# Performance work log

Measured on AMD Instinct MI355X. Metric: run time of the kernel, lower is better.

The kernel has to match this reference:

```python
import jax, jax.numpy as jnp
import numpy as np

B, T, C = 2, 2048, 1024
H, HS = 16, 64
THETA = 10000.0


def _rope_tables(seq_len, dim, dtype):
    inv_freq = 1.0 / (THETA ** (jnp.arange(0, dim, 2, dtype=jnp.float32) / dim))
    t = jnp.arange(seq_len, dtype=jnp.float32)
    freqs = t[:, None] * inv_freq[None, :]          # [T, dim/2]
    emb = jnp.concatenate([freqs, freqs], axis=-1)  # [T, dim]
    return jnp.cos(emb).astype(dtype), jnp.sin(emb).astype(dtype)


def _rotate_half(x):
    x1, x2 = jnp.split(x, 2, axis=-1)
    return jnp.concatenate([-x2, x1], axis=-1)


def setup_inputs() -> dict:
    key = jax.random.key(0)
    ks = jax.random.split(key, 9)
    s = 0.02
    return {
        "q_x": jax.random.normal(ks[0], (B, T, C), dtype=jnp.float32),
        "wq": jax.random.normal(ks[1], (C, H * HS), dtype=jnp.float32) * s,
        "bq": jnp.zeros((H * HS,), dtype=jnp.float32),
        "wk": jax.random.normal(ks[2], (C, H * HS), dtype=jnp.float32) * s,
        "bk": jnp.zeros((H * HS,), dtype=jnp.float32),
        "wv": jax.random.normal(ks[3], (C, H * HS), dtype=jnp.float32) * s,
        "bv": jnp.zeros((H * HS,), dtype=jnp.float32),
        "wc": jax.random.normal(ks[4], (H * HS, C), dtype=jnp.float32) * s,
        "bc": jnp.zeros((C,), dtype=jnp.float32),
    }


def reference(q_x, wq, bq, wk, bk, wv, bv, wc, bc):
    b, t, _ = q_x.shape
    # Q/K/V projections -> [B, H, T, HS]
    q = (q_x @ wq + bq).reshape(b, t, H, HS).transpose(0, 2, 1, 3)
    k = (q_x @ wk + bk).reshape(b, t, H, HS).transpose(0, 2, 1, 3)
    v = (q_x @ wv + bv).reshape(b, t, H, HS).transpose(0, 2, 1, 3)
    # RoPE (concat-half rotation)
    cos, sin = _rope_tables(t, HS, q.dtype)  # [T, HS]
    q = q * cos + _rotate_half(q) * sin
    k = k * cos + _rotate_half(k) * sin
    # Naive causal attention
    scale = 1.0 / np.sqrt(HS)
    att = jnp.einsum("bhqd,bhkd->bhqk", q, k) * scale
    mask = jnp.tril(jnp.ones((t, t), dtype=bool))
    att = jnp.where(mask, att, -jnp.inf)
    att = jax.nn.softmax(att, axis=-1)
    y = jnp.einsum("bhqk,bhkd->bhqd", att, v)
    y = y.transpose(0, 2, 1, 3).reshape(b, t, H * HS)
    return y @ wc + bc
```

## Files before the change

### kernel.cpp

```cpp
#include <hip/hip_runtime.h>

#define B_  2
#define T_  2048
#define C_  1024
#define H_  16
#define HS_ 64
#define M_  4096
#define N_  1024
#define K_  1024

typedef float floatx4 __attribute__((ext_vector_type(4)));
typedef short bf16x8  __attribute__((ext_vector_type(8)));

__device__ __forceinline__ float bf2f(unsigned short u) {
    return __uint_as_float(((unsigned int)u) << 16);
}
__device__ __forceinline__ unsigned short f2bf(float f) {
    unsigned int u = __float_as_uint(f);
    return (unsigned short)((u + 0x7fffu + ((u >> 16) & 1u)) >> 16);
}
__device__ __forceinline__ unsigned int pack2(float a, float b) {
    return (unsigned int)f2bf(a) | ((unsigned int)f2bf(b) << 16);
}
__device__ __forceinline__ unsigned int pack2t(float a, float b) {
    return __builtin_amdgcn_perm(__float_as_uint(b), __float_as_uint(a), 0x07060302u);
}
__device__ __forceinline__ void async16(const unsigned short* g, unsigned short* l) {
    __builtin_amdgcn_global_load_lds(
        (const __attribute__((address_space(1))) unsigned int*)g,
        (__attribute__((address_space(3))) unsigned int*)l, 16, 0, 0);
}

__global__ __launch_bounds__(256) void prep_kernel(
    const float* __restrict__ x,
    const float* __restrict__ w0, const float* __restrict__ w1,
    const float* __restrict__ w2, const float* __restrict__ w3,
    unsigned short* __restrict__ xb, unsigned short* __restrict__ wTall)
{
    __shared__ float tile[64][65];
    const int bid = blockIdx.x;
    const int t = threadIdx.x;
    if (bid < 4096) {
        const size_t i = ((size_t)bid * 256 + t) * 4;
        const float4 v = *(const float4*)(x + i);
        ushort4 st;
        st.x = f2bf(v.x); st.y = f2bf(v.y); st.z = f2bf(v.z); st.w = f2bf(v.w);
        *(ushort4*)(xb + i) = st;
        return;
    }
    const int zb = bid - 4096;
    const int z = zb >> 8, rem = zb & 255;
    const float* w = (z == 0) ? w0 : (z == 1) ? w1 : (z == 2) ? w2 : w3;
    unsigned short* wT = wTall + ((size_t)z << 20);
    const int n0 = (rem & 15) * 64, k0 = (rem >> 4) * 64;

    const int r = t >> 2, cq = (t & 3) * 16;
    const float4* src = (const float4*)(w + (size_t)(k0 + r) * N_ + n0 + cq);
    const float4 v0 = src[0], v1 = src[1], v2 = src[2], v3 = src[3];
    tile[r][cq+0]=v0.x; tile[r][cq+1]=v0.y; tile[r][cq+2]=v0.z; tile[r][cq+3]=v0.w;
    tile[r][cq+4]=v1.x; tile[r][cq+5]=v1.y; tile[r][cq+6]=v1.z; tile[r][cq+7]=v1.w;
    tile[r][cq+8]=v2.x; tile[r][cq+9]=v2.y; tile[r][cq+10]=v2.z; tile[r][cq+11]=v2.w;
    tile[r][cq+12]=v3.x; tile[r][cq+13]=v3.y; tile[r][cq+14]=v3.z; tile[r][cq+15]=v3.w;
    __syncthreads();

    const int rn = t >> 2, ck = (t & 3) * 16;
    unsigned int o[8];
#pragma unroll
    for (int ii = 0; ii < 8; ii++)
        o[ii] = pack2(tile[ck + 2*ii][rn], tile[ck + 2*ii + 1][rn]);
    unsigned short* dst = wT + (size_t)(n0 + rn) * K_ + k0 + ck;
    *(uint4*)dst       = make_uint4(o[0], o[1], o[2], o[3]);
    *(uint4*)(dst + 8) = make_uint4(o[4], o[5], o[6], o[7]);
}

__global__ __launch_bounds__(512, 2) void qkv_gemm(
    const unsigned short* __restrict__ xb, const unsigned short* __restrict__ wT,
    const float* __restrict__ bq, const float* __restrict__ bk,
    const float* __restrict__ bv,
    unsigned short* __restrict__ qb, unsigned short* __restrict__ kb,
    unsigned short* __restrict__ vb)
{
    __shared__ unsigned short lds[65536];

    const int tid  = threadIdx.x;
    const int lane = tid & 63;
    const int wave = tid >> 6;

    const int bid = blockIdx.x;
    const int swz = (bid & 7) * 24 + (bid >> 3);
    const int nb  = swz % 12;
    const int mb  = swz / 12;
    const int m0  = mb * 256;
    const int n0g = nb * 256;

    const int wm = wave >> 2, wn = wave & 3;
    const int fr = lane & 15, quad = lane >> 4;

    const int r_s = tid >> 2;
    const int c_s = (tid & 3) ^ ((tid >> 3) & 3);
    const unsigned short* aS0 = xb + (size_t)(m0 + r_s) * 1024 + c_s * 8;
    const unsigned short* aS1 = aS0 + (size_t)128 * 1024;
    const unsigned short* bS0 = wT + (size_t)(n0g + r_s) * 1024 + c_s * 8;
    const unsigned short* bS1 = bS0 + (size_t)128 * 1024;
    unsigned short* ldw = &lds[wave * 512];

    auto stage = [&](int buf, int region, const unsigned short* s0,
                     const unsigned short* s1) {
        unsigned short* d = ldw + buf * 32768 + region * 8192;
        async16(s0, d);
        async16(s1, d + 4096);
    };

    int oA[8], oB[4];
#pragma unroll
    for (int i = 0; i < 8; i++) {
        const int r = wm * 128 + i * 16 + fr;
        oA[i] = r * 32 + ((quad ^ ((r >> 1) & 3)) << 3);
    }
#pragma unroll
    for (int j = 0; j < 4; j++) {
        const int r = wn * 64 + j * 16 + fr;
        oB[j] = r * 32 + ((quad ^ ((r >> 1) & 3)) << 3);
    }

    floatx4 acc[8][4];
#pragma unroll
    for (int i = 0; i < 8; i++)
#pragma unroll
        for (int j = 0; j < 4; j++) acc[i][j] = (floatx4){0.f, 0.f, 0.f, 0.f};

    stage(0, 0, aS0,      aS1);
    stage(0, 2, bS0,      bS1);
    stage(0, 1, aS0 + 32, aS1 + 32);
    stage(0, 3, bS0 + 32, bS1 + 32);
    stage(1, 0, aS0 + 64, aS1 + 64);
    stage(1, 2, bS0 + 64, bS1 + 64);
    asm volatile("s_waitcnt vmcnt(8)" ::: "memory");
    __builtin_amdgcn_s_barrier();
    __builtin_amdgcn_sched_barrier(0);

    bf16x8 af[4], bfr[4];
#pragma unroll 2
    for (int t = 0; t < 16; ++t) {
        const int cur = t & 1, nxt = cur ^ 1;
        const unsigned short* A0 = &lds[cur * 32768];
        const unsigned short* A1 = A0 + 8192;
        const unsigned short* B0 = A0 + 16384;
        const unsigned short* B1 = A0 + 24576;
        const int k1 = (t + 1) * 64, k2 = (t + 2) * 64;

#pragma unroll
        for (int i = 0; i < 4; i++) af[i]  = *(const bf16x8*)&A0[oA[i]];
#pragma unroll
        for (int j = 0; j < 4; j++) bfr[j] = *(const bf16x8*)&B0[oB[j]];
        if (t + 1 < 16) stage(nxt, 1, aS0 + k1 + 32, aS1 + k1 + 32);
        __builtin_amdgcn_s_barrier();
        asm volatile("s_waitcnt lgkmcnt(0)" ::: "memory");
        __builtin_amdgcn_s_setprio(1);
#pragma unroll
        for (int i = 0; i < 4; i++)
#pragma unroll
            for (int j = 0; j < 4; j++)
                acc[i][j] = __builtin_amdgcn_mfma_f32_16x16x32_bf16(
                    af[i], bfr[j], acc[i][j], 0, 0, 0);
        __builtin_amdgcn_s_setprio(0);
        __builtin_amdgcn_s_barrier();
        __builtin_amdgcn_sched_barrier(0);

#pragma unroll
        for (int i = 0; i < 4; i++) af[i] = *(const bf16x8*)&A0[oA[4 + i]];
        if (t + 1 < 16) stage(nxt, 3, bS0 + k1 + 32, bS1 + k1 + 32);
        if (t < 15) { asm volatile("s_waitcnt vmcnt(8)" ::: "memory"); }
        else        { asm volatile("s_waitcnt vmcnt(0)" ::: "memory"); }
        __builtin_amdgcn_s_barrier();
        asm volatile("s_waitcnt lgkmcnt(0)" ::: "memory");
        __builtin_amdgcn_s_setprio(1);
#pragma unroll
        for (int i = 0; i < 4; i++)
#pragma unroll
            for (int j = 0; j < 4; j++)
                acc[4 + i][j] = __builtin_amdgcn_mfma_f32_16x16x32_bf16(
                    af[i], bfr[j], acc[4 + i][j], 0, 0, 0);
        __builtin_amdgcn_s_setprio(0);
        __builtin_amdgcn_s_barrier();
        __builtin_amdgcn_sched_barrier(0);

#pragma unroll
        for (int i = 0; i < 4; i++) af[i]  = *(const bf16x8*)&A1[oA[i]];
#pragma unroll
        for (int j = 0; j < 4; j++) bfr[j] = *(const bf16x8*)&B1[oB[j]];
        if (t + 2 < 16) stage(cur, 0, aS0 + k2, aS1 + k2);
        __builtin_amdgcn_s_barrier();
        asm volatile("s_waitcnt lgkmcnt(0)" ::: "memory");
        __builtin_amdgcn_s_setprio(1);
#pragma unroll
        for (int i = 0; i < 4; i++)
#pragma unroll
            for (int j = 0; j < 4; j++)
                acc[i][j] = __builtin_amdgcn_mfma_f32_16x16x32_bf16(
                    af[i], bfr[j], acc[i][j], 0, 0, 0);
        __builtin_amdgcn_s_setprio(0);
        __builtin_amdgcn_s_barrier();
        __builtin_amdgcn_sched_barrier(0);

#pragma unroll
        for (int i = 0; i < 4; i++) af[i] = *(const bf16x8*)&A1[oA[4 + i]];
        if (t + 2 < 16) stage(cur, 2, bS0 + k2, bS1 + k2);
        if (t < 14) { asm volatile("s_waitcnt vmcnt(8)" ::: "memory"); }
        else        { asm volatile("s_waitcnt vmcnt(0)" ::: "memory"); }
        __builtin_amdgcn_s_barrier();
        asm volatile("s_waitcnt lgkmcnt(0)" ::: "memory");
        __builtin_amdgcn_s_setprio(1);
#pragma unroll
        for (int i = 0; i < 4; i++)
#pragma unroll
            for (int j = 0; j < 4; j++)
                acc[4 + i][j] = __builtin_amdgcn_mfma_f32_16x16x32_bf16(
                    af[i], bfr[j], acc[4 + i][j], 0, 0, 0);
        __builtin_amdgcn_s_setprio(0);
        __builtin_amdgcn_s_barrier();
        __builtin_amdgcn_sched_barrier(0);
    }

    const int p = nb >> 2;
    const int colbase = (nb & 3) * 256 + wn * 64;
    const int h = colbase >> 6;
    const int rb = quad * 4;
    const float* bias = (p == 0) ? bq : (p == 1) ? bk : bv;

    if (p == 2) {
#pragma unroll
        for (int j = 0; j < 4; j++) {
            const int d = j * 16 + fr;
            const float bz = bias[colbase + d];
#pragma unroll
            for (int i = 0; i < 8; i++) {
                const int row0 = m0 + wm * 128 + i * 16 + rb;
                const int bb = row0 >> 11, tt = row0 & 2047;
                ushort4 st;
                st.x = f2bf(acc[i][j][0] + bz);
                st.y = f2bf(acc[i][j][1] + bz);
                st.z = f2bf(acc[i][j][2] + bz);
                st.w = f2bf(acc[i][j][3] + bz);
                *(ushort4*)&vb[((size_t)(bb * H_ + h) * HS_ + d) * T_ + tt] = st;
            }
        }
    } else {
        unsigned short* out = (p == 0) ? qb : kb;
        const float qsc = (p == 0) ? 0.18033688011111772f : 1.0f;
        const float bz0 = bias[colbase + fr];
        const float bz1 = bias[colbase + 16 + fr];
        const float bz2 = bias[colbase + 32 + fr];
        const float bz3 = bias[colbase + 48 + fr];
        const float nl = -0.41524101186279297f;
        const float if0 = exp2f((float)fr * nl);
        const float if1 = exp2f((float)(fr + 16) * nl);
#pragma unroll
        for (int i = 0; i < 8; i++) {
#pragma unroll
            for (int pr = 0; pr < 4; pr++) {
                const int row = m0 + wm * 128 + i * 16 + rb + pr;
                const int bb = row >> 11, tt = row & 2047;
                float s0, c0, s1, c1;
                __sincosf((float)tt * if0, &s0, &c0);
                __sincosf((float)tt * if1, &s1, &c1);
                const float v0 = acc[i][0][pr] + bz0;
                const float v1 = acc[i][1][pr] + bz1;
                const float v2 = acc[i][2][pr] + bz2;
                const float v3 = acc[i][3][pr] + bz3;
                unsigned short* ob = out + ((size_t)(bb * H_ + h) * T_ + tt) * HS_ + fr;
                ob[0]  = f2bf((v0 * c0 - v2 * s0) * qsc);
                ob[16] = f2bf((v1 * c1 - v3 * s1) * qsc);
                ob[32] = f2bf((v2 * c0 + v0 * s0) * qsc);
                ob[48] = f2bf((v3 * c1 + v1 * s1) * qsc);
            }
        }
    }
}

__global__ __launch_bounds__(256) void attn_kernel(
    const unsigned short* __restrict__ qb, const unsigned short* __restrict__ kb,
    const unsigned short* __restrict__ vt, unsigned short* __restrict__ yb,
    unsigned short* __restrict__ Opart, float* __restrict__ Mpart)
{
    __shared__ unsigned short Ks[2][64 * 64];
    __shared__ unsigned short Vs[2][64 * 64];
    __shared__ unsigned short Ps[4][16 * 64];

    const int bh = blockIdx.x;
    const int b = bh >> 4, h = bh & 15;
    const int s = 47 - (int)blockIdx.y;
    int qt, ktlo, kthi, half;
    bool split;
    if (s < 16) { qt = s; ktlo = 0; kthi = qt; half = 0; split = false; }
    else {
        const int idx = s - 16;
        qt = 16 + (idx >> 1); half = idx & 1;
        const int nf = (qt + 2) >> 1;
        ktlo = half ? nf : 0;
        kthi = half ? qt : nf - 1;
        split = true;
    }
    const int r0 = qt * 64;
    const int tid  = threadIdx.x;
    const int lane = tid & 63;
    const int wave = tid >> 6;
    const int l4   = lane & 15;
    const int quad = lane >> 4;

    const int qrow_g = r0 + wave * 16 + l4;

    bf16x8 qf[2];
    {
        const unsigned short* qp = qb + ((size_t)bh * T_ + qrow_g) * HS_ + quad * 8;
        qf[0] = *(const bf16x8*)(qp);
        qf[1] = *(const bf16x8*)(qp + 32);
    }

    floatx4 o[4];
#pragma unroll
    for (int g = 0; g < 4; g++) o[g] = (floatx4){0.f, 0.f, 0.f, 0.f};
    float m = -1e30f, l = 0.f;

    const int srow = tid >> 2;
    const int sc16 = (tid & 3) * 16;
    const int ssw  = (srow & 7) * 8;
    const int psw  = (l4 & 7) * 8;

    const unsigned short* kp = kb + ((size_t)bh * T_ + srow) * HS_ + sc16;
    const unsigned short* vp = vt + ((size_t)(bh * 64 + srow)) * T_ + sc16;

    uint4 rk0 = *(const uint4*)(kp + (size_t)ktlo * 64 * HS_);
    uint4 rk1 = *(const uint4*)(kp + (size_t)ktlo * 64 * HS_ + 8);
    uint4 rv0 = *(const uint4*)(vp + ktlo * 64);
    uint4 rv1 = *(const uint4*)(vp + ktlo * 64 + 8);
    *(uint4*)&Ks[0][srow * 64 + ( sc16      ^ ssw)] = rk0;
    *(uint4*)&Ks[0][srow * 64 + ((sc16 + 8) ^ ssw)] = rk1;
    *(uint4*)&Vs[0][srow * 64 + ( sc16      ^ ssw)] = rv0;
    *(uint4*)&Vs[0][srow * 64 + ((sc16 + 8) ^ ssw)] = rv1;

    for (int kt = ktlo; kt <= kthi; kt++) {
        const int cur = (kt - ktlo) & 1;
        if (kt < kthi) {
            const unsigned short* kpn = kp + (size_t)(kt + 1) * (64 * HS_);
            const unsigned short* vpn = vp + (kt + 1) * 64;
            rk0 = *(const uint4*)kpn;
            rk1 = *(const uint4*)(kpn + 8);
            rv0 = *(const uint4*)vpn;
            rv1 = *(const uint4*)(vpn + 8);
        }
        __syncthreads();

        floatx4 sf[4];
        __builtin_amdgcn_s_setprio(1);
#pragma unroll
        for (int mg = 0; mg < 4; mg++) {
            const int key = mg * 16 + l4;
            const int ksw = (key & 7) * 8;
            const bf16x8 a0 = *(const bf16x8*)&Ks[cur][key * 64 + ( (quad * 8)       ^ ksw)];
            const bf16x8 a1 = *(const bf16x8*)&Ks[cur][key * 64 + (((quad * 8) + 32) ^ ksw)];
            floatx4 z = (floatx4){0.f, 0.f, 0.f, 0.f};
            z = __builtin_amdgcn_mfma_f32_16x16x32_bf16(a0, qf[0], z, 0, 0, 0);
            z = __builtin_amdgcn_mfma_f32_16x16x32_bf16(a1, qf[1], z, 0, 0, 0);
            sf[mg] = z;
        }
        __builtin_amdgcn_s_setprio(0);

        if (kt == qt) {
#pragma unroll
            for (int mg = 0; mg < 4; mg++)
#pragma unroll
                for (int r = 0; r < 4; r++)
                    if (kt * 64 + 16 * mg + quad * 4 + r > qrow_g)
                        sf[mg][r] = -1e30f;
        }

        float mx[4];
#pragma unroll
        for (int mg = 0; mg < 4; mg++)
            mx[mg] = fmaxf(fmaxf(sf[mg][0], sf[mg][1]),
                           fmaxf(sf[mg][2], sf[mg][3]));
        float tm = fmaxf(fmaxf(mx[0], mx[1]), fmaxf(mx[2], mx[3]));

        if (!__all(tm <= m + 8.f)) {
            tm = fmaxf(tm, __shfl_xor(tm, 16));
            tm = fmaxf(tm, __shfl_xor(tm, 32));
            const float mnew  = fmaxf(m, tm);
            const float alpha = __builtin_amdgcn_exp2f(m - mnew);
            l *= alpha;
#pragma unroll
            for (int g = 0; g < 4; g++) o[g] = o[g] * alpha;
            m = mnew;
        }

        float p[4][4];
        float psg[4];
#pragma unroll
        for (int mg = 0; mg < 4; mg++) {
#pragma unroll
            for (int r = 0; r < 4; r++)
                p[mg][r] = __builtin_amdgcn_exp2f(sf[mg][r] - m);
            psg[mg] = (p[mg][0] + p[mg][1]) + (p[mg][2] + p[mg][3]);
        }
        l += (psg[0] + psg[1]) + (psg[2] + psg[3]);

#pragma unroll
        for (int mg = 0; mg < 4; mg++) {
            const int kb4 = 16 * mg + quad * 4;
            const int off = ((kb4 & ~7) ^ psw) | (kb4 & 7);
            uint2 w;
            w.x = pack2t(p[mg][0], p[mg][1]);
            w.y = pack2t(p[mg][2], p[mg][3]);
            *(uint2*)&Ps[wave][l4 * 64 + off] = w;
        }

        const bf16x8 pf0 = *(const bf16x8*)&Ps[wave][l4 * 64 + ( (quad * 8)       ^ psw)];
        const bf16x8 pf1 = *(const bf16x8*)&Ps[wave][l4 * 64 + (((quad * 8) + 32) ^ psw)];
        __builtin_amdgcn_s_setprio(1);
#pragma unroll
        for (int g = 0; g < 4; g++) {
            const int vd  = g * 16 + l4;
            const int vsw = (vd & 7) * 8;
            const bf16x8 va0 = *(const bf16x8*)&Vs[cur][vd * 64 + ( (quad * 8)       ^ vsw)];
            const bf16x8 va1 = *(const bf16x8*)&Vs[cur][vd * 64 + (((quad * 8) + 32) ^ vsw)];
            o[g] = __builtin_amdgcn_mfma_f32_16x16x32_bf16(va0, pf0, o[g], 0, 0, 0);
            o[g] = __builtin_amdgcn_mfma_f32_16x16x32_bf16(va1, pf1, o[g], 0, 0, 0);
        }
        __builtin_amdgcn_s_setprio(0);

        if (kt < kthi) {
            const int nxt = cur ^ 1;
            *(uint4*)&Ks[nxt][srow * 64 + ( sc16      ^ ssw)] = rk0;
            *(uint4*)&Ks[nxt][srow * 64 + ((sc16 + 8) ^ ssw)] = rk1;
            *(uint4*)&Vs[nxt][srow * 64 + ( sc16      ^ ssw)] = rv0;
            *(uint4*)&Vs[nxt][srow * 64 + ((sc16 + 8) ^ ssw)] = rv1;
        }
    }

    l += __shfl_xor(l, 16);
    l += __shfl_xor(l, 32);

    if (!split) {
        const float invl = 1.f / l;
        unsigned short* yrow = yb + ((size_t)(b * T_ + qrow_g) * H_ + h) * HS_;
#pragma unroll
        for (int g = 0; g < 4; g++) {
            ushort4 st;
            st.x = f2bf(o[g][0] * invl);
            st.y = f2bf(o[g][1] * invl);
            st.z = f2bf(o[g][2] * invl);
            st.w = f2bf(o[g][3] * invl);
            *(ushort4*)&yrow[16 * g + quad * 4] = st;
        }
    } else {
        const int u  = (bh * 16 + (qt - 16)) * 2 + half;
        const int rl = wave * 16 + l4;
        unsigned short* Op = Opart + (size_t)u * 4096 + rl * 64;
#pragma unroll
        for (int g = 0; g < 4; g++) {
            ushort4 st;
            st.x = f2bf(o[g][0]);
            st.y = f2bf(o[g][1]);
            st.z = f2bf(o[g][2]);
            st.w = f2bf(o[g][3]);
            *(ushort4*)&Op[16 * g + quad * 4] = st;
        }
        if (quad == 0) {
            float* ml = Mpart + (size_t)u * 128;
            ml[rl]      = m;
            ml[64 + rl] = l;
        }
    }
}

__global__ __launch_bounds__(256) void attn_combine(
    const unsigned short* __restrict__ Opart, const float* __restrict__ Mpart,
    unsigned short* __restrict__ yb)
{
    const int u  = blockIdx.x;
    const int bh = u >> 4, qt = 16 + (u & 15);
    const int b = bh >> 4, h = bh & 15;
    const int t = threadIdx.x;
    const int r = t >> 2, c = (t & 3) * 16;

    const float* ml1 = Mpart + (size_t)(u * 2) * 128;
    const float* ml2 = ml1 + 128;
    const float m1 = ml1[r], l1 = ml1[64 + r];
    const float m2 = ml2[r], l2 = ml2[64 + r];
    const float M  = fmaxf(m1, m2);
    const float w1 = __builtin_amdgcn_exp2f(m1 - M);
    const float w2 = __builtin_amdgcn_exp2f(m2 - M);
    const float inv = 1.f / (l1 * w1 + l2 * w2);
    const float a1 = w1 * inv, a2 = w2 * inv;

    const unsigned short* O1 = Opart + (size_t)(u * 2)     * 4096 + r * 64 + c;
    const unsigned short* O2 = Opart + (size_t)(u * 2 + 1) * 4096 + r * 64 + c;
    unsigned short* yrow = yb + ((size_t)(b * T_ + qt * 64 + r) * H_ + h) * HS_ + c;

#pragma unroll
    for (int j = 0; j < 2; j++) {
        const uint4 u1 = *(const uint4*)(O1 + 8 * j);
        const uint4 u2 = *(const uint4*)(O2 + 8 * j);
        const unsigned int a[4] = {u1.x, u1.y, u1.z, u1.w};
        const unsigned int d[4] = {u2.x, u2.y, u2.z, u2.w};
        unsigned int ov[4];
#pragma unroll
        for (int q = 0; q < 4; q++) {
            const float y0 = bf2f((unsigned short)(a[q] & 0xffff)) * a1
                           + bf2f((unsigned short)(d[q] & 0xffff)) * a2;
            const float y1 = bf2f((unsigned short)(a[q] >> 16)) * a1
                           + bf2f((unsigned short)(d[q] >> 16)) * a2;
            ov[q] = pack2(y0, y1);
        }
        *(uint4*)(yrow + 8 * j) = make_uint4(ov[0], ov[1], ov[2], ov[3]);
    }
}

__global__ __launch_bounds__(256, 2) void out_gemm(
    const unsigned short* __restrict__ A, const unsigned short* __restrict__ wcT,
    const float* __restrict__ bias, float* __restrict__ out)
{
    __shared__ unsigned short lds[32768];

    const int tid  = threadIdx.x;
    const int lane = tid & 63;
    const int wave = tid >> 6;

    const int bid = blockIdx.x;
    const int swz = (bid & 7) * 32 + (bid >> 3);
    const int nt  = swz >> 5;
    const int mt  = swz & 31;
    const int m0  = mt * 128;
    const int n0  = nt * 128;

    const int wm = wave >> 1, wn = wave & 1;
    const int fr = lane & 15, quad = lane >> 4;

    const int r_s = tid >> 2;
    const int c_s = (tid & 3) ^ ((tid >> 3) & 3);
    const unsigned short* aS0 = A   + (size_t)(m0 + r_s) * 1024 + c_s * 8;
    const unsigned short* aS1 = aS0 + (size_t)64 * 1024;
    const unsigned short* bS0 = wcT + (size_t)(n0 + r_s) * 1024 + c_s * 8;
    const unsigned short* bS1 = bS0 + (size_t)64 * 1024;
    unsigned short* ldw = &lds[wave * 512];

    auto stage = [&](int buf, int region, const unsigned short* s0,
                     const unsigned short* s1) {
        unsigned short* d = ldw + buf * 16384 + region * 4096;
        async16(s0, d);
        async16(s1, d + 2048);
    };

    int oA[4], oB[4];
#pragma unroll
    for (int i = 0; i < 4; i++) {
        const int r = wm * 64 + i * 16 + fr;
        oA[i] = r * 32 + ((quad ^ ((r >> 1) & 3)) << 3);
    }
#pragma unroll
    for (int j = 0; j < 4; j++) {
        const int r = wn * 64 + j * 16 + fr;
        oB[j] = r * 32 + ((quad ^ ((r >> 1) & 3)) << 3);
    }

    floatx4 acc[4][4];
#pragma unroll
    for (int i = 0; i < 4; i++)
#pragma unroll
        for (int j = 0; j < 4; j++) acc[i][j] = (floatx4){0.f, 0.f, 0.f, 0.f};

    stage(0, 0, aS0,      aS1);
    stage(0, 2, bS0,      bS1);
    stage(0, 1, aS0 + 32, aS1 + 32);
    stage(0, 3, bS0 + 32, bS1 + 32);
    stage(1, 0, aS0 + 64, aS1 + 64);
    stage(1, 2, bS0 + 64, bS1 + 64);
    asm volatile("s_waitcnt vmcnt(8)" ::: "memory");
    __builtin_amdgcn_s_barrier();
    __builtin_amdgcn_sched_barrier(0);

    bf16x8 af[2], bfr[4];
#pragma unroll 2
    for (int t = 0; t < 16; ++t) {
        const int cur = t & 1, nxt = cur ^ 1;
        const unsigned short* A0 = &lds[cur * 16384];
        const unsigned short* A1 = A0 + 4096;
        const unsigned short* B0 = A0 + 8192;
        const unsigned short* B1 = A0 + 12288;
        const int k1 = (t + 1) * 64, k2 = (t + 2) * 64;

#pragma unroll
        for (int i = 0; i < 2; i++) af[i]  = *(const bf16x8*)&A0[oA[i]];
#pragma unroll
        for (int j = 0; j < 4; j++) bfr[j] = *(const bf16x8*)&B0[oB[j]];
        if (t + 1 < 16) stage(nxt, 1, aS0 + k1 + 32, aS1 + k1 + 32);
        __builtin_amdgcn_s_barrier();
        asm volatile("s_waitcnt lgkmcnt(0)" ::: "memory");
        __builtin_amdgcn_s_setprio(1);
#pragma unroll
        for (int i = 0; i < 2; i++)
#pragma unroll
            for (int j = 0; j < 4; j++)
                acc[i][j] = __builtin_amdgcn_mfma_f32_16x16x32_bf16(
                    af[i], bfr[j], acc[i][j], 0, 0, 0);
        __builtin_amdgcn_s_setprio(0);
        __builtin_amdgcn_s_barrier();
        __builtin_amdgcn_sched_barrier(0);

#pragma unroll
        for (int i = 0; i < 2; i++) af[i] = *(const bf16x8*)&A0[oA[2 + i]];
        if (t + 1 < 16) stage(nxt, 3, bS0 + k1 + 32, bS1 + k1 + 32);
        if (t < 15) { asm volatile("s_waitcnt vmcnt(8)" ::: "memory"); }
        else        { asm volatile("s_waitcnt vmcnt(0)" ::: "memory"); }
        __builtin_amdgcn_s_barrier();
        asm volatile("s_waitcnt lgkmcnt(0)" ::: "memory");
        __builtin_amdgcn_s_setprio(1);
#pragma unroll
        for (int i = 0; i < 2; i++)
#pragma unroll
            for (int j = 0; j < 4; j++)
                acc[2 + i][j] = __builtin_amdgcn_mfma_f32_16x16x32_bf16(
                    af[i], bfr[j], acc[2 + i][j], 0, 0, 0);
        __builtin_amdgcn_s_setprio(0);
        __builtin_amdgcn_s_barrier();
        __builtin_amdgcn_sched_barrier(0);

#pragma unroll
        for (int i = 0; i < 2; i++) af[i]  = *(const bf16x8*)&A1[oA[i]];
#pragma unroll
        for (int j = 0; j < 4; j++) bfr[j] = *(const bf16x8*)&B1[oB[j]];
        if (t + 2 < 16) stage(cur, 0, aS0 + k2, aS1 + k2);
        __builtin_amdgcn_s_barrier();
        asm volatile("s_waitcnt lgkmcnt(0)" ::: "memory");
        __builtin_amdgcn_s_setprio(1);
#pragma unroll
        for (int i = 0; i < 2; i++)
#pragma unroll
            for (int j = 0; j < 4; j++)
                acc[i][j] = __builtin_amdgcn_mfma_f32_16x16x32_bf16(
                    af[i], bfr[j], acc[i][j], 0, 0, 0);
        __builtin_amdgcn_s_setprio(0);
        __builtin_amdgcn_s_barrier();
        __builtin_amdgcn_sched_barrier(0);

#pragma unroll
        for (int i = 0; i < 2; i++) af[i] = *(const bf16x8*)&A1[oA[2 + i]];
        if (t + 2 < 16) stage(cur, 2, bS0 + k2, bS1 + k2);
        if (t < 14) { asm volatile("s_waitcnt vmcnt(8)" ::: "memory"); }
        else        { asm volatile("s_waitcnt vmcnt(0)" ::: "memory"); }
        __builtin_amdgcn_s_barrier();
        asm volatile("s_waitcnt lgkmcnt(0)" ::: "memory");
        __builtin_amdgcn_s_setprio(1);
#pragma unroll
        for (int i = 0; i < 2; i++)
#pragma unroll
            for (int j = 0; j < 4; j++)
                acc[2 + i][j] = __builtin_amdgcn_mfma_f32_16x16x32_bf16(
                    af[i], bfr[j], acc[2 + i][j], 0, 0, 0);
        __builtin_amdgcn_s_setprio(0);
        __builtin_amdgcn_s_barrier();
        __builtin_amdgcn_sched_barrier(0);
    }

    const int rbase = quad * 4;
#pragma unroll
    for (int j = 0; j < 4; j++) {
        const int col = n0 + wn * 64 + j * 16 + fr;
        const float bz = bias[col];
#pragma unroll
        for (int i = 0; i < 4; i++) {
#pragma unroll
            for (int pr = 0; pr < 4; pr++) {
                const int row = m0 + wm * 64 + i * 16 + rbase + pr;
                out[(size_t)row * N_ + col] = acc[i][j][pr] + bz;
            }
        }
    }
}

extern "C" void kernel_launch(void* const* d_in, const int* in_sizes, int n_in,
                              void* d_out, int out_size, void* d_ws, size_t ws_size,
                              hipStream_t stream) {
    const float* x  = (const float*)d_in[0];
    const float* wq = (const float*)d_in[1];
    const float* bq = (const float*)d_in[2];
    const float* wk = (const float*)d_in[3];
    const float* bk = (const float*)d_in[4];
    const float* wv = (const float*)d_in[5];
    const float* bv = (const float*)d_in[6];
    const float* wc = (const float*)d_in[7];
    const float* bc = (const float*)d_in[8];
    float* out = (float*)d_out;

    unsigned short* ws  = (unsigned short*)d_ws;
    unsigned short* qb  = ws;
    unsigned short* kb  = ws + (size_t)4194304;
    unsigned short* vb  = ws + (size_t)8388608;
    unsigned short* yb  = ws + (size_t)12582912;
    unsigned short* xb  = ws + (size_t)16777216;
    unsigned short* wT  = ws + (size_t)20971520;
    unsigned short* wcT = wT + ((size_t)3 << 20);
    unsigned short* Opart = xb;
    float*          Mpart = (float*)wT;

    prep_kernel<<<5120, 256, 0, stream>>>(x, wq, wk, wv, wc, xb, wT);
    qkv_gemm<<<192, 512, 0, stream>>>(xb, wT, bq, bk, bv, qb, kb, vb);
    attn_kernel<<<dim3(32, 48), 256, 0, stream>>>(qb, kb, vb, yb, Opart, Mpart);
    attn_combine<<<512, 256, 0, stream>>>(Opart, Mpart, yb);
    out_gemm<<<256, 256, 0, stream>>>(yb, wcT, bc, out);
}
```

Measured before the change: 188.0 us.

## Widen attention key/value tiles to 128 keys per iteration

Each loop iteration in the attention kernel now stages 128 keys of K and V into shared memory instead of 64. It computes two 64-key score blocks and feeds them through the softmax and PV MFMA in two halves. This halves the number of barrier-synchronised iterations and per-iteration overheads such as the max reduction and rescale check. The split-KV boundaries and the causal diagonal tile index are recomputed for the wider tiles. It doubles shared memory for K/V and register staging, which may reduce occupancy, and it computes more masked work on the diagonal tile.

```diff
diff --git a/kernel.cpp b/kernel.cpp
--- a/kernel.cpp
+++ b/kernel.cpp
@@ -283,8 +283,8 @@
     const unsigned short* __restrict__ vt, unsigned short* __restrict__ yb,
     unsigned short* __restrict__ Opart, float* __restrict__ Mpart)
 {
-    __shared__ unsigned short Ks[2][64 * 64];
-    __shared__ unsigned short Vs[2][64 * 64];
+    __shared__ unsigned short Ks[2][128 * 64];
+    __shared__ unsigned short Vs[2][64 * 128];
     __shared__ unsigned short Ps[4][16 * 64];
 
     const int bh = blockIdx.x;
@@ -292,15 +292,18 @@
     const int s = 47 - (int)blockIdx.y;
     int qt, ktlo, kthi, half;
     bool split;
-    if (s < 16) { qt = s; ktlo = 0; kthi = qt; half = 0; split = false; }
-    else {
+    if (s < 16) {
+        qt = s; ktlo = 0; kthi = ((qt + 2) >> 1) - 1; half = 0; split = false;
+    } else {
         const int idx = s - 16;
         qt = 16 + (idx >> 1); half = idx & 1;
-        const int nf = (qt + 2) >> 1;
+        const int n  = (qt + 2) >> 1;
+        const int nf = (n + 1) >> 1;
         ktlo = half ? nf : 0;
-        kthi = half ? qt : nf - 1;
+        kthi = half ? n - 1 : nf - 1;
         split = true;
     }
+    const int kdiag = ((qt + 2) >> 1) - 1;
     const int r0 = qt * 64;
     const int tid  = threadIdx.x;
     const int lane = tid & 63;
@@ -330,57 +333,82 @@
     const unsigned short* kp = kb + ((size_t)bh * T_ + srow) * HS_ + sc16;
     const unsigned short* vp = vt + ((size_t)(bh * 64 + srow)) * T_ + sc16;
 
-    uint4 rk0 = *(const uint4*)(kp + (size_t)ktlo * 64 * HS_);
-    uint4 rk1 = *(const uint4*)(kp + (size_t)ktlo * 64 * HS_ + 8);
-    uint4 rv0 = *(const uint4*)(vp + ktlo * 64);
-    uint4 rv1 = *(const uint4*)(vp + ktlo * 64 + 8);
-    *(uint4*)&Ks[0][srow * 64 + ( sc16      ^ ssw)] = rk0;
-    *(uint4*)&Ks[0][srow * 64 + ((sc16 + 8) ^ ssw)] = rk1;
-    *(uint4*)&Vs[0][srow * 64 + ( sc16      ^ ssw)] = rv0;
-    *(uint4*)&Vs[0][srow * 64 + ((sc16 + 8) ^ ssw)] = rv1;
+    uint4 rk0, rk1, rk2, rk3, rv0, rv1, rv2, rv3;
+    {
+        const unsigned short* kpt = kp + (size_t)ktlo * (128 * HS_);
+        rk0 = *(const uint4*)(kpt);
+        rk1 = *(const uint4*)(kpt + 8);
+        rk2 = *(const uint4*)(kpt + 64 * HS_);
+        rk3 = *(const uint4*)(kpt + 64 * HS_ + 8);
+        const unsigned short* vpt = vp + ktlo * 128;
+        rv0 = *(const uint4*)(vpt);
+        rv1 = *(const uint4*)(vpt + 8);
+        rv2 = *(const uint4*)(vpt + 64);
+        rv3 = *(const uint4*)(vpt + 72);
+    }
+    *(uint4*)&Ks[0][ srow       * 64 + ( sc16       ^ ssw)] = rk0;
+    *(uint4*)&Ks[0][ srow       * 64 + ((sc16 + 8)  ^ ssw)] = rk1;
+    *(uint4*)&Ks[0][(srow + 64) * 64 + ( sc16       ^ ssw)] = rk2;
+    *(uint4*)&Ks[0][(srow + 64) * 64 + ((sc16 + 8)  ^ ssw)] = rk3;
+    *(uint4*)&Vs[0][ srow * 128 + ( sc16       ^ ssw)] = rv0;
+    *(uint4*)&Vs[0][ srow * 128 + ((sc16 + 8)  ^ ssw)] = rv1;
+    *(uint4*)&Vs[0][ srow * 128 + ((sc16 + 64) ^ ssw)] = rv2;
+    *(uint4*)&Vs[0][ srow * 128 + ((sc16 + 72) ^ ssw)] = rv3;
 
     for (int kt = ktlo; kt <= kthi; kt++) {
         const int cur = (kt - ktlo) & 1;
         if (kt < kthi) {
-            const unsigned short* kpn = kp + (size_t)(kt + 1) * (64 * HS_);
-            const unsigned short* vpn = vp + (kt + 1) * 64;
+            const unsigned short* kpn = kp + (size_t)(kt + 1) * (128 * HS_);
             rk0 = *(const uint4*)kpn;
             rk1 = *(const uint4*)(kpn + 8);
+            rk2 = *(const uint4*)(kpn + 64 * HS_);
+            rk3 = *(const uint4*)(kpn + 64 * HS_ + 8);
+            const unsigned short* vpn = vp + (kt + 1) * 128;
             rv0 = *(const uint4*)vpn;
             rv1 = *(const uint4*)(vpn + 8);
+            rv2 = *(const uint4*)(vpn + 64);
+            rv3 = *(const uint4*)(vpn + 72);
         }
         __syncthreads();
 
-        floatx4 sf[4];
-        __builtin_amdgcn_s_setprio(1);
+        floatx4 sf[2][4];
+        __builtin_amdgcn_s_setprio(1);
+#pragma unroll
+        for (int hh = 0; hh < 2; hh++)
 #pragma unroll
         for (int mg = 0; mg < 4; mg++) {
-            const int key = mg * 16 + l4;
+            const int key = hh * 64 + mg * 16 + l4;
             const int ksw = (key & 7) * 8;
             const bf16x8 a0 = *(const bf16x8*)&Ks[cur][key * 64 + ( (quad * 8)       ^ ksw)];
             const bf16x8 a1 = *(const bf16x8*)&Ks[cur][key * 64 + (((quad * 8) + 32) ^ ksw)];
             floatx4 z = (floatx4){0.f, 0.f, 0.f, 0.f};
             z = __builtin_amdgcn_mfma_f32_16x16x32_bf16(a0, qf[0], z, 0, 0, 0);
             z = __builtin_amdgcn_mfma_f32_16x16x32_bf16(a1, qf[1], z, 0, 0, 0);
-            sf[mg] = z;
-        }
-        __builtin_amdgcn_s_setprio(0);
-
-        if (kt == qt) {
+            sf[hh][mg] = z;
+        }
+        __builtin_amdgcn_s_setprio(0);
+
+        if (kt == kdiag) {
+#pragma unroll
+            for (int hh = 0; hh < 2; hh++)
 #pragma unroll
             for (int mg = 0; mg < 4; mg++)
 #pragma unroll
                 for (int r = 0; r < 4; r++)
-                    if (kt * 64 + 16 * mg + quad * 4 + r > qrow_g)
-                        sf[mg][r] = -1e30f;
-        }
-
-        float mx[4];
+                    if (kt * 128 + hh * 64 + 16 * mg + quad * 4 + r > qrow_g)
+                        sf[hh][mg][r] = -1e30f;
+        }
+
+        float mxg[8];
+#pragma unroll
+        for (int hh = 0; hh < 2; hh++)
 #pragma unroll
         for (int mg = 0; mg < 4; mg++)
-            mx[mg] = fmaxf(fmaxf(sf[mg][0], sf[mg][1]),
-                           fmaxf(sf[mg][2], sf[mg][3]));
-        float tm = fmaxf(fmaxf(mx[0], mx[1]), fmaxf(mx[2], mx[3]));
+            mxg[hh * 4 + mg] = fmaxf(fmaxf(sf[hh][mg][0], sf[hh][mg][1]),
+                                     fmaxf(sf[hh][mg][2], sf[hh][mg][3]));
+        const float m01 = fmaxf(mxg[0], mxg[1]), m23 = fmaxf(mxg[2], mxg[3]);
+        const float m45 = fmaxf(mxg[4], mxg[5]), m67 = fmaxf(mxg[6], mxg[7]);
+        float tm = fmaxf(fmaxf(m01, m23), fmaxf(m45, m67));
 
         if (!__all(tm <= m + 8.f)) {
             tm = fmaxf(tm, __shfl_xor(tm, 16));
@@ -393,47 +421,54 @@
             m = mnew;
         }
 
-        float p[4][4];
-        float psg[4];
-#pragma unroll
-        for (int mg = 0; mg < 4; mg++) {
-#pragma unroll
-            for (int r = 0; r < 4; r++)
-                p[mg][r] = __builtin_amdgcn_exp2f(sf[mg][r] - m);
-            psg[mg] = (p[mg][0] + p[mg][1]) + (p[mg][2] + p[mg][3]);
-        }
-        l += (psg[0] + psg[1]) + (psg[2] + psg[3]);
-
-#pragma unroll
-        for (int mg = 0; mg < 4; mg++) {
-            const int kb4 = 16 * mg + quad * 4;
-            const int off = ((kb4 & ~7) ^ psw) | (kb4 & 7);
-            uint2 w;
-            w.x = pack2t(p[mg][0], p[mg][1]);
-            w.y = pack2t(p[mg][2], p[mg][3]);
-            *(uint2*)&Ps[wave][l4 * 64 + off] = w;
-        }
-
-        const bf16x8 pf0 = *(const bf16x8*)&Ps[wave][l4 * 64 + ( (quad * 8)       ^ psw)];
-        const bf16x8 pf1 = *(const bf16x8*)&Ps[wave][l4 * 64 + (((quad * 8) + 32) ^ psw)];
-        __builtin_amdgcn_s_setprio(1);
-#pragma unroll
-        for (int g = 0; g < 4; g++) {
-            const int vd  = g * 16 + l4;
-            const int vsw = (vd & 7) * 8;
-            const bf16x8 va0 = *(const bf16x8*)&Vs[cur][vd * 64 + ( (quad * 8)       ^ vsw)];
-            const bf16x8 va1 = *(const bf16x8*)&Vs[cur][vd * 64 + (((quad * 8) + 32) ^ vsw)];
-            o[g] = __builtin_amdgcn_mfma_f32_16x16x32_bf16(va0, pf0, o[g], 0, 0, 0);
-            o[g] = __builtin_amdgcn_mfma_f32_16x16x32_bf16(va1, pf1, o[g], 0, 0, 0);
-        }
-        __builtin_amdgcn_s_setprio(0);
+#pragma unroll
+        for (int hh = 0; hh < 2; hh++) {
+            float pq[4][4];
+            float ls = 0.f;
+#pragma unroll
+            for (int mg = 0; mg < 4; mg++) {
+#pragma unroll
+                for (int r = 0; r < 4; r++)
+                    pq[mg][r] = __builtin_amdgcn_exp2f(sf[hh][mg][r] - m);
+                ls += (pq[mg][0] + pq[mg][1]) + (pq[mg][2] + pq[mg][3]);
+            }
+            l += ls;
+
+#pragma unroll
+            for (int mg = 0; mg < 4; mg++) {
+                const int kb4 = 16 * mg + quad * 4;
+                const int off = ((kb4 & ~7) ^ psw) | (kb4 & 7);
+                uint2 w;
+                w.x = pack2t(pq[mg][0], pq[mg][1]);
+                w.y = pack2t(pq[mg][2], pq[mg][3]);
+                *(uint2*)&Ps[wave][l4 * 64 + off] = w;
+            }
+
+            const bf16x8 pf0 = *(const bf16x8*)&Ps[wave][l4 * 64 + ( (quad * 8)       ^ psw)];
+            const bf16x8 pf1 = *(const bf16x8*)&Ps[wave][l4 * 64 + (((quad * 8) + 32) ^ psw)];
+            __builtin_amdgcn_s_setprio(1);
+#pragma unroll
+            for (int g = 0; g < 4; g++) {
+                const int vd  = g * 16 + l4;
+                const int vsw = (vd & 7) * 8;
+                const bf16x8 va0 = *(const bf16x8*)&Vs[cur][vd * 128 + ((hh * 64 + quad * 8)      ^ vsw)];
+                const bf16x8 va1 = *(const bf16x8*)&Vs[cur][vd * 128 + ((hh * 64 + quad * 8 + 32) ^ vsw)];
+                o[g] = __builtin_amdgcn_mfma_f32_16x16x32_bf16(va0, pf0, o[g], 0, 0, 0);
+                o[g] = __builtin_amdgcn_mfma_f32_16x16x32_bf16(va1, pf1, o[g], 0, 0, 0);
+            }
+            __builtin_amdgcn_s_setprio(0);
+        }
 
         if (kt < kthi) {
             const int nxt = cur ^ 1;
-            *(uint4*)&Ks[nxt][srow * 64 + ( sc16      ^ ssw)] = rk0;
-            *(uint4*)&Ks[nxt][srow * 64 + ((sc16 + 8) ^ ssw)] = rk1;
-            *(uint4*)&Vs[nxt][srow * 64 + ( sc16      ^ ssw)] = rv0;
-            *(uint4*)&Vs[nxt][srow * 64 + ((sc16 + 8) ^ ssw)] = rv1;
+            *(uint4*)&Ks[nxt][ srow       * 64 + ( sc16       ^ ssw)] = rk0;
+            *(uint4*)&Ks[nxt][ srow       * 64 + ((sc16 + 8)  ^ ssw)] = rk1;
+            *(uint4*)&Ks[nxt][(srow + 64) * 64 + ( sc16       ^ ssw)] = rk2;
+            *(uint4*)&Ks[nxt][(srow + 64) * 64 + ((sc16 + 8)  ^ ssw)] = rk3;
+            *(uint4*)&Vs[nxt][ srow * 128 + ( sc16       ^ ssw)] = rv0;
+            *(uint4*)&Vs[nxt][ srow * 128 + ((sc16 + 8)  ^ ssw)] = rv1;
+            *(uint4*)&Vs[nxt][ srow * 128 + ((sc16 + 64) ^ ssw)] = rv2;
+            *(uint4*)&Vs[nxt][ srow * 128 + ((sc16 + 72) ^ ssw)] = rv3;
         }
     }
 
```

After: 191.0 us. Within noise of the previous version (+1.6%).
